# Optimization experiments

Hardware: AMD Instinct MI355X
Metric: run time of the kernel (lower is better)

The kernel has to match this reference:

```python
import jax, jax.numpy as jnp
import numpy as np

N = 100000   # nodes
E = 1600000  # edges
G = 64       # graphs in batch
C = 8        # num_classes
H = 128      # hidden dim


def _lin(k, out_f, in_f):
    return jax.random.normal(k, (out_f, in_f), jnp.float32) * (1.0 / np.sqrt(in_f))


def setup_inputs() -> dict:
    key = jax.random.key(0)
    ks = jax.random.split(key, 16)
    x = jax.random.normal(ks[0], (N, 5), jnp.float32)
    edge_index = jax.random.randint(ks[1], (2, E), 0, N)
    batch = jnp.sort(jax.random.randint(ks[2], (N,), 0, G))
    exinfo = jax.random.normal(ks[3], (G, 10), jnp.float32)
    return {
        "x": x, "edge_index": edge_index, "batch": batch, "exinfo": exinfo,
        # GraphConv1: 3 -> 128 (PyG GraphConv: lin_root(x) + lin_rel(scatter_add(x_j)))
        "Wroot1": _lin(ks[4], H, 3), "Wrel1": _lin(ks[5], H, 3), "brel1": jnp.zeros((H,), jnp.float32),
        # GraphConv2: 128 -> 128
        "Wroot2": _lin(ks[6], H, H), "Wrel2": _lin(ks[7], H, H), "brel2": jnp.zeros((H,), jnp.float32),
        # MLP head
        "W1": _lin(ks[8], 64, 2 * H + 10), "b1": jnp.zeros((64,), jnp.float32),
        "W2": _lin(ks[9], 32, 64), "b2": jnp.zeros((32,), jnp.float32),
        "W3": _lin(ks[10], C, 32), "b3": jnp.zeros((C,), jnp.float32),
    }


def _graph_conv(x, src, dst, Wroot, Wrel, brel):
    # PyG GraphConv (aggr='add'): out_i = Wrel @ sum_{j->i} x_j + brel + Wroot @ x_i
    agg = jax.ops.segment_sum(x[src], dst, num_segments=x.shape[0])  # [N, F]
    return agg @ Wrel.T + brel + x @ Wroot.T


def reference(x, edge_index, batch, exinfo,
              Wroot1, Wrel1, brel1, Wroot2, Wrel2, brel2,
              W1, b1, W2, b2, W3, b3):
    xs = x[:, 2:5]                              # data.x[:, 2:5]
    src, dst = edge_index[0], edge_index[1]
    x1 = jax.nn.relu(_graph_conv(xs, src, dst, Wroot1, Wrel1, brel1))   # [N, 128]
    x2 = jax.nn.relu(_graph_conv(x1, src, dst, Wroot2, Wrel2, brel2))   # [N, 128]
    h = jnp.concatenate([x1, x2], axis=-1)      # [N, 256]
    g = jax.ops.segment_max(h, batch, num_segments=G)  # global max pool [G, 256]
    g = jnp.concatenate([g, exinfo], axis=-1)   # [G, 266]
    g = jax.nn.relu(g @ W1.T + b1)
    g = jax.nn.relu(g @ W2.T + b2)
    return jax.nn.log_softmax(g @ W3.T + b3, axis=-1)
```

## Files before the change

kernel.cpp:

```cpp
#include <hip/hip_runtime.h>

#define N_NODES 100000
#define N_EDGES 1600000
#define NG 64
#define NC 8
#define HD 128

#define BUCKET_SHIFT 8
#define NB ((N_NODES + 255) >> 8)
#define NCHUNK 256
#define EPC (N_EDGES / NCHUNK)

typedef __attribute__((ext_vector_type(8))) __bf16 bf16x8;
typedef __attribute__((ext_vector_type(4))) float f32x4;


__global__ void bin_hist_k(const int* __restrict__ dst, int* __restrict__ hist) {
  __shared__ int lh[NB];
  int c = blockIdx.x, t = threadIdx.x;
  for (int b = t; b < NB; b += 256) lh[b] = 0;
  __syncthreads();
  int e0 = c * EPC;
  for (int i = t; i < EPC; i += 256) atomicAdd(&lh[dst[e0 + i] >> BUCKET_SHIFT], 1);
  __syncthreads();
  for (int b = t; b < NB; b += 256) hist[c * NB + b] = lh[b];
}

__launch_bounds__(512)
__global__ void base_k(const int* __restrict__ hist, int* __restrict__ bucket_base,
                       int* __restrict__ row_ptr) {
  __shared__ int tot[512];
  int t = threadIdx.x;
  int s = 0;
  if (t < NB)
    for (int c = 0; c < NCHUNK; c++) s += hist[c * NB + t];
  tot[t] = s;
  __syncthreads();
  for (int off = 1; off < 512; off <<= 1) {
    int v = (t >= off) ? tot[t - off] : 0;
    __syncthreads();
    tot[t] += v;
    __syncthreads();
  }
  if (t < NB) bucket_base[t] = tot[t] - s;
  if (t == 0) { bucket_base[NB] = N_EDGES; row_ptr[N_NODES] = N_EDGES; }
}

__global__ void chunk_scan_k(int* __restrict__ hist, const int* __restrict__ bucket_base) {
  int b = blockIdx.x, lane = threadIdx.x;
  int carry = bucket_base[b];
#pragma unroll
  for (int it = 0; it < NCHUNK / 64; it++) {
    int c = it * 64 + lane;
    int v = hist[c * NB + b];
    int s = v;
#pragma unroll
    for (int off = 1; off < 64; off <<= 1) {
      int u = __shfl_up(s, off);
      if (lane >= off) s += u;
    }
    hist[c * NB + b] = carry + s - v;
    carry += __shfl(s, 63);
  }
}

__global__ void scatter_k(const int* __restrict__ src, const int* __restrict__ dst,
                          const int* __restrict__ hist, int2* __restrict__ pairs) {
  __shared__ int loff[NB];
  int c = blockIdx.x, t = threadIdx.x;
  for (int b = t; b < NB; b += 256) loff[b] = hist[c * NB + b];
  __syncthreads();
  int e0 = c * EPC;
  for (int i = t; i < EPC; i += 256) {
    int d = dst[e0 + i], s = src[e0 + i];
    int pos = atomicAdd(&loff[d >> BUCKET_SHIFT], 1);
    pairs[pos] = make_int2(d, s);
  }
}

__global__ void bucket_csr_k(const int2* __restrict__ pairs,
                             const int* __restrict__ bucket_base,
                             int* __restrict__ row_ptr, int* __restrict__ csr) {
  __shared__ int cnt[256];
  __shared__ int start[256];
  __shared__ int wsum[4];
  int b = blockIdx.x, t = threadIdx.x, lane = t & 63, wid = t >> 6;
  int nb0 = b << BUCKET_SHIFT;
  int beg = bucket_base[b], end = bucket_base[b + 1];
  cnt[t] = 0;
  __syncthreads();
  for (int i = beg + t; i < end; i += 256) atomicAdd(&cnt[pairs[i].x - nb0], 1);
  __syncthreads();
  int v = cnt[t];
  int s = v;
#pragma unroll
  for (int off = 1; off < 64; off <<= 1) {
    int u = __shfl_up(s, off);
    if (lane >= off) s += u;
  }
  if (lane == 63) wsum[wid] = s;
  __syncthreads();
  if (t == 0) {
    int a = 0;
    for (int j = 0; j < 4; j++) { int x = wsum[j]; wsum[j] = a; a += x; }
  }
  __syncthreads();
  int excl = wsum[wid] + s - v;
  start[t] = excl;
  if (nb0 + t < N_NODES) row_ptr[nb0 + t] = beg + excl;
  cnt[t] = 0;
  __syncthreads();
  for (int i = beg + t; i < end; i += 256) {
    int2 p = pairs[i];
    int li = p.x - nb0;
    int pos = beg + start[li] + atomicAdd(&cnt[li], 1);
    csr[pos] = p.y;
  }
}


__global__ void conv1_k(const float* __restrict__ x, const int* __restrict__ row_ptr,
                        const int* __restrict__ csr, const float* __restrict__ Wroot1,
                        const float* __restrict__ Wrel1, const float* __restrict__ brel1,
                        __bf16* __restrict__ xcat) {
  int node = blockIdx.x * 4 + (threadIdx.x >> 6);
  if (node >= N_NODES) return;
  int lane = threadIdx.x & 63;
  int beg = row_ptr[node], end = row_ptr[node + 1];
  float a0 = 0.f, a1 = 0.f, a2 = 0.f;
  for (int e = beg + lane; e < end; e += 64) {
    int s = csr[e];
    const float* xp = x + (size_t)s * 5;
    a0 += xp[2]; a1 += xp[3]; a2 += xp[4];
  }
#pragma unroll
  for (int m = 1; m < 64; m <<= 1) {
    a0 += __shfl_xor(a0, m);
    a1 += __shfl_xor(a1, m);
    a2 += __shfl_xor(a2, m);
  }
  const float* xn = x + (size_t)node * 5;
  float r0 = xn[2], r1 = xn[3], r2 = xn[4];
  __bf16* orow = xcat + (size_t)node * 256 + 128;
#pragma unroll
  for (int hh = 0; hh < 2; hh++) {
    int h = lane + hh * 64;
    float v = brel1[h]
            + a0 * Wrel1[h * 3 + 0] + a1 * Wrel1[h * 3 + 1] + a2 * Wrel1[h * 3 + 2]
            + r0 * Wroot1[h * 3 + 0] + r1 * Wroot1[h * 3 + 1] + r2 * Wroot1[h * 3 + 2];
    orow[h] = (__bf16)fmaxf(v, 0.f);
  }
}


__global__ void agg2_k(const int* __restrict__ row_ptr, const int* __restrict__ csr,
                       __bf16* xcat) {
  int node = blockIdx.x * 4 + (threadIdx.x >> 6);
  if (node >= N_NODES) return;
  int lane = threadIdx.x & 63;
  int g = lane >> 4, f = lane & 15;
  int beg = row_ptr[node], end = row_ptr[node + 1];
  int deg = end - beg;
  int idx = (lane < deg) ? csr[beg + lane] : 0;
  float acc[8];
#pragma unroll
  for (int k = 0; k < 8; k++) acc[k] = 0.f;
  int dmain = deg < 64 ? deg : 64;
  int j = 0;
  for (; j + 8 <= dmain; j += 8) {
    int s0 = __shfl(idx, j + g);
    int s1 = __shfl(idx, j + 4 + g);
    uint4 u0 = *((const uint4*)(xcat + (size_t)s0 * 256 + 128) + f);
    uint4 u1 = *((const uint4*)(xcat + (size_t)s1 * 256 + 128) + f);
    acc[0] += __uint_as_float(u0.x << 16);  acc[1] += __uint_as_float(u0.x & 0xffff0000u);
    acc[2] += __uint_as_float(u0.y << 16);  acc[3] += __uint_as_float(u0.y & 0xffff0000u);
    acc[4] += __uint_as_float(u0.z << 16);  acc[5] += __uint_as_float(u0.z & 0xffff0000u);
    acc[6] += __uint_as_float(u0.w << 16);  acc[7] += __uint_as_float(u0.w & 0xffff0000u);
    acc[0] += __uint_as_float(u1.x << 16);  acc[1] += __uint_as_float(u1.x & 0xffff0000u);
    acc[2] += __uint_as_float(u1.y << 16);  acc[3] += __uint_as_float(u1.y & 0xffff0000u);
    acc[4] += __uint_as_float(u1.z << 16);  acc[5] += __uint_as_float(u1.z & 0xffff0000u);
    acc[6] += __uint_as_float(u1.w << 16);  acc[7] += __uint_as_float(u1.w & 0xffff0000u);
  }
  for (; j + 4 <= dmain; j += 4) {
    int s0 = __shfl(idx, j + g);
    uint4 u0 = *((const uint4*)(xcat + (size_t)s0 * 256 + 128) + f);
    acc[0] += __uint_as_float(u0.x << 16);  acc[1] += __uint_as_float(u0.x & 0xffff0000u);
    acc[2] += __uint_as_float(u0.y << 16);  acc[3] += __uint_as_float(u0.y & 0xffff0000u);
    acc[4] += __uint_as_float(u0.z << 16);  acc[5] += __uint_as_float(u0.z & 0xffff0000u);
    acc[6] += __uint_as_float(u0.w << 16);  acc[7] += __uint_as_float(u0.w & 0xffff0000u);
  }
  {
    int rem = dmain - j;
    int s0 = __shfl(idx, j + (g < rem ? g : 0));
    if (g < rem) {
      uint4 u0 = *((const uint4*)(xcat + (size_t)s0 * 256 + 128) + f);
      acc[0] += __uint_as_float(u0.x << 16);  acc[1] += __uint_as_float(u0.x & 0xffff0000u);
      acc[2] += __uint_as_float(u0.y << 16);  acc[3] += __uint_as_float(u0.y & 0xffff0000u);
      acc[4] += __uint_as_float(u0.z << 16);  acc[5] += __uint_as_float(u0.z & 0xffff0000u);
      acc[6] += __uint_as_float(u0.w << 16);  acc[7] += __uint_as_float(u0.w & 0xffff0000u);
    }
  }
  for (int e = beg + 64; e < end; e += 4) {
    int m = end - e;
    int s0 = csr[e + (g < m ? g : 0)];
    if (g < m) {
      uint4 u0 = *((const uint4*)(xcat + (size_t)s0 * 256 + 128) + f);
      acc[0] += __uint_as_float(u0.x << 16);  acc[1] += __uint_as_float(u0.x & 0xffff0000u);
      acc[2] += __uint_as_float(u0.y << 16);  acc[3] += __uint_as_float(u0.y & 0xffff0000u);
      acc[4] += __uint_as_float(u0.z << 16);  acc[5] += __uint_as_float(u0.z & 0xffff0000u);
      acc[6] += __uint_as_float(u0.w << 16);  acc[7] += __uint_as_float(u0.w & 0xffff0000u);
    }
  }
#pragma unroll
  for (int k = 0; k < 8; k++) {
    acc[k] += __shfl_xor(acc[k], 16);
    acc[k] += __shfl_xor(acc[k], 32);
  }
  if (g == 0) {
    uint4 o;
    o.x = (__float_as_uint((float)(__bf16)acc[0]) >> 16) | (__float_as_uint((float)(__bf16)acc[1]) & 0xffff0000u);
    o.y = (__float_as_uint((float)(__bf16)acc[2]) >> 16) | (__float_as_uint((float)(__bf16)acc[3]) & 0xffff0000u);
    o.z = (__float_as_uint((float)(__bf16)acc[4]) >> 16) | (__float_as_uint((float)(__bf16)acc[5]) & 0xffff0000u);
    o.w = (__float_as_uint((float)(__bf16)acc[6]) >> 16) | (__float_as_uint((float)(__bf16)acc[7]) & 0xffff0000u);
    *((uint4*)(xcat + (size_t)node * 256) + f) = o;
  }
}


__global__ void build_wc_k(const float* __restrict__ Wrel2, const float* __restrict__ Wroot2,
                           __bf16* __restrict__ Wc) {
  int i = blockIdx.x * 256 + threadIdx.x;
  int h = i >> 8, k = i & 255;
  float v = (k < 128) ? Wrel2[h * 128 + k] : Wroot2[h * 128 + (k - 128)];
  Wc[i] = (__bf16)v;
}


__launch_bounds__(256)
__global__ void gemm2_k(const __bf16* __restrict__ xcat, const __bf16* __restrict__ Wc,
                        const float* __restrict__ brel2, __bf16* __restrict__ x2) {
  int wid = threadIdx.x >> 6, lane = threadIdx.x & 63;
  int nb = (blockIdx.x * 4 + wid) * 32;
  if (nb >= N_NODES) return;
  int r = lane & 15, ko = lane >> 4;
  const __bf16* arow0 = xcat + (size_t)(nb + r) * 256 + ko * 8;
  const __bf16* arow1 = arow0 + 16 * 256;
  const __bf16* brow = Wc + (size_t)r * 256 + ko * 8;
  f32x4 acc0[8], acc1[8];
#pragma unroll
  for (int i = 0; i < 8; i++) {
    acc0[i] = (f32x4){0.f, 0.f, 0.f, 0.f};
    acc1[i] = (f32x4){0.f, 0.f, 0.f, 0.f};
  }
#pragma unroll
  for (int kb = 0; kb < 256; kb += 32) {
    bf16x8 a0 = *(const bf16x8*)(arow0 + kb);
    bf16x8 a1 = *(const bf16x8*)(arow1 + kb);
#pragma unroll
    for (int ht = 0; ht < 8; ht++) {
      bf16x8 b = *(const bf16x8*)(brow + (size_t)ht * 16 * 256 + kb);
      acc0[ht] = __builtin_amdgcn_mfma_f32_16x16x32_bf16(a0, b, acc0[ht], 0, 0, 0);
      acc1[ht] = __builtin_amdgcn_mfma_f32_16x16x32_bf16(a1, b, acc1[ht], 0, 0, 0);
    }
  }
#pragma unroll
  for (int ht = 0; ht < 8; ht++) {
    int h = ht * 16 + r;
    float bias = brel2[h];
#pragma unroll
    for (int rr = 0; rr < 4; rr++) {
      int node = nb + ko * 4 + rr;
      x2[(size_t)node * 128 + h] = (__bf16)fmaxf(acc0[ht][rr] + bias, 0.f);
      x2[(size_t)(node + 16) * 128 + h] = (__bf16)fmaxf(acc1[ht][rr] + bias, 0.f);
    }
  }
}


__global__ void segmax_k(const __bf16* __restrict__ xcat, const __bf16* __restrict__ x2,
                         const int* __restrict__ batch, unsigned int* __restrict__ g) {
  int t = threadIdx.x;
  int n0 = blockIdx.x * 128;
  if (n0 >= N_NODES) return;
  int n1 = n0 + 128 < N_NODES ? n0 + 128 : N_NODES;
  int cur = batch[n0];
  float m = 0.f;
  for (int n = n0; n < n1; n++) {
    int b = batch[n];
    if (b != cur) {
      atomicMax(&g[cur * 256 + t], __float_as_uint(m));
      cur = b; m = 0.f;
    }
    float v = (t < 128) ? (float)xcat[(size_t)n * 256 + 128 + t]
                        : (float)x2[(size_t)n * 128 + (t - 128)];
    m = fmaxf(m, v);
  }
  atomicMax(&g[cur * 256 + t], __float_as_uint(m));
}


__global__ void head1_k(const float* __restrict__ g, const float* __restrict__ exinfo,
                        const float* __restrict__ W1, const float* __restrict__ b1,
                        float* __restrict__ g1) {
  int gg = blockIdx.x;
  int t = threadIdx.x;
  int c = t >> 2, q = t & 3;
  const float* w = W1 + c * 266;
  const float* gr = g + gg * 256;
  float s = 0.f;
  for (int k = q * 64; k < q * 64 + 64; k++) s += gr[k] * w[k];
  if (q == 0) {
    const float* er = exinfo + gg * 10;
    for (int k = 0; k < 10; k++) s += er[k] * w[256 + k];
    s += b1[c];
  }
  s += __shfl_xor(s, 1);
  s += __shfl_xor(s, 2);
  if (q == 0) g1[gg * 64 + c] = fmaxf(s, 0.f);
}

__global__ void head2_k(const float* __restrict__ g1, const float* __restrict__ W2,
                        const float* __restrict__ b2, const float* __restrict__ W3,
                        const float* __restrict__ b3, float* __restrict__ out) {
  __shared__ float s1[64 * 64];
  __shared__ float s2[64 * 32];
  int t = threadIdx.x;
  for (int i = t; i < 4096; i += 256) s1[i] = g1[i];
  __syncthreads();
  for (int o = t; o < 2048; o += 256) {
    int r = o >> 5, c = o & 31;
    float s = b2[c];
    for (int k = 0; k < 64; k++) s += s1[r * 64 + k] * W2[c * 64 + k];
    s2[r * 32 + c] = fmaxf(s, 0.f);
  }
  __syncthreads();
  if (t < 64) {
    float lg[8];
#pragma unroll
    for (int c = 0; c < 8; c++) {
      float s = b3[c];
      for (int k = 0; k < 32; k++) s += s2[t * 32 + k] * W3[c * 32 + k];
      lg[c] = s;
    }
    float mx = lg[0];
#pragma unroll
    for (int c = 1; c < 8; c++) mx = fmaxf(mx, lg[c]);
    float se = 0.f;
#pragma unroll
    for (int c = 0; c < 8; c++) se += expf(lg[c] - mx);
    float lse = mx + logf(se);
#pragma unroll
    for (int c = 0; c < 8; c++) out[t * 8 + c] = lg[c] - lse;
  }
}


extern "C" void kernel_launch(void* const* d_in, const int* in_sizes, int n_in,
                              void* d_out, int out_size, void* d_ws, size_t ws_size,
                              hipStream_t stream) {
  const float* x      = (const float*)d_in[0];
  const int*   edge   = (const int*)d_in[1];
  const int*   batch  = (const int*)d_in[2];
  const float* exinfo = (const float*)d_in[3];
  const float* Wroot1 = (const float*)d_in[4];
  const float* Wrel1  = (const float*)d_in[5];
  const float* brel1  = (const float*)d_in[6];
  const float* Wroot2 = (const float*)d_in[7];
  const float* Wrel2  = (const float*)d_in[8];
  const float* brel2  = (const float*)d_in[9];
  const float* W1     = (const float*)d_in[10];
  const float* b1     = (const float*)d_in[11];
  const float* W2     = (const float*)d_in[12];
  const float* b2     = (const float*)d_in[13];
  const float* W3     = (const float*)d_in[14];
  const float* b3     = (const float*)d_in[15];
  const int* src = edge;
  const int* dst = edge + N_EDGES;

  char* p = (char*)d_ws;
  auto alloc = [&](size_t bytes) {
    char* q = p;
    p += (bytes + 511) & ~(size_t)511;
    return (void*)q;
  };
  __bf16*       Wc          = (__bf16*)alloc(128 * 256 * 2);
  unsigned int* g           = (unsigned int*)alloc(64 * 256 * 4);
  float*        g1          = (float*)alloc(64 * 64 * 4);
  int*          hist        = (int*)alloc((size_t)NCHUNK * NB * 4);
  int*          bucket_base = (int*)alloc((size_t)(NB + 1) * 4);
  int*          row_ptr     = (int*)alloc((size_t)(N_NODES + 1) * 4);
  int*          csr         = (int*)alloc((size_t)N_EDGES * 4);
  __bf16*       xcat        = (__bf16*)alloc((size_t)N_NODES * 256 * 2);
  void*         xp2         = alloc((size_t)N_NODES * 128 * 2);
  int2*         pairs       = (int2*)xp2;
  __bf16*       x2          = (__bf16*)xp2;

  hipMemsetAsync(g, 0, 64 * 256 * 4, stream);
  build_wc_k<<<128, 256, 0, stream>>>(Wrel2, Wroot2, Wc);
  bin_hist_k<<<NCHUNK, 256, 0, stream>>>(dst, hist);
  base_k<<<1, 512, 0, stream>>>(hist, bucket_base, row_ptr);
  chunk_scan_k<<<NB, 64, 0, stream>>>(hist, bucket_base);
  scatter_k<<<NCHUNK, 256, 0, stream>>>(src, dst, hist, pairs);
  bucket_csr_k<<<NB, 256, 0, stream>>>(pairs, bucket_base, row_ptr, csr);
  conv1_k<<<25000, 256, 0, stream>>>(x, row_ptr, csr, Wroot1, Wrel1, brel1, xcat);
  agg2_k<<<25000, 256, 0, stream>>>(row_ptr, csr, xcat);
  gemm2_k<<<782, 256, 0, stream>>>(xcat, Wc, brel2, x2);
  segmax_k<<<782, 256, 0, stream>>>(xcat, x2, batch, g);
  head1_k<<<64, 256, 0, stream>>>((const float*)g, exinfo, W1, b1, g1);
  head2_k<<<1, 256, 0, stream>>>(g1, W2, b2, W3, b3, (float*)d_out);
}
```

Before: 246.4 us.

## Fuse second-layer max-pool into GEMM epilogue and unroll edge gather deeper

The GEMM epilogue for the second GraphConv now applies bias and ReLU and reduces each 32-node tile straight into the per-graph max buffer with atomics. This removes the materialised x2 tensor and its later re-read. A separate segmax kernel now covers only the first-layer half of the features, reading packed bf16 pairs with four node strides per block. The neighbor-aggregation loop is unrolled to four outstanding row loads per iteration to raise memory-level parallelism. The cost is more atomics to global memory when a tile spans a graph boundary, and higher register pressure in the gather.

```diff
diff --git a/kernel.cpp b/kernel.cpp
--- a/kernel.cpp
+++ b/kernel.cpp
@@ -153,6 +153,13 @@
 }
 
 
+#define LDROW(s) (*((const uint4*)(xcat + (size_t)(s) * 256 + 128) + f))
+#define ACC8(u) \
+  acc[0] += __uint_as_float((u).x << 16);  acc[1] += __uint_as_float((u).x & 0xffff0000u); \
+  acc[2] += __uint_as_float((u).y << 16);  acc[3] += __uint_as_float((u).y & 0xffff0000u); \
+  acc[4] += __uint_as_float((u).z << 16);  acc[5] += __uint_as_float((u).z & 0xffff0000u); \
+  acc[6] += __uint_as_float((u).w << 16);  acc[7] += __uint_as_float((u).w & 0xffff0000u);
+
 __global__ void agg2_k(const int* __restrict__ row_ptr, const int* __restrict__ csr,
                        __bf16* xcat) {
   int node = blockIdx.x * 4 + (threadIdx.x >> 6);
@@ -167,48 +174,45 @@
   for (int k = 0; k < 8; k++) acc[k] = 0.f;
   int dmain = deg < 64 ? deg : 64;
   int j = 0;
-  for (; j + 8 <= dmain; j += 8) {
+  for (; j + 16 <= dmain; j += 16) {
     int s0 = __shfl(idx, j + g);
     int s1 = __shfl(idx, j + 4 + g);
-    uint4 u0 = *((const uint4*)(xcat + (size_t)s0 * 256 + 128) + f);
-    uint4 u1 = *((const uint4*)(xcat + (size_t)s1 * 256 + 128) + f);
-    acc[0] += __uint_as_float(u0.x << 16);  acc[1] += __uint_as_float(u0.x & 0xffff0000u);
-    acc[2] += __uint_as_float(u0.y << 16);  acc[3] += __uint_as_float(u0.y & 0xffff0000u);
-    acc[4] += __uint_as_float(u0.z << 16);  acc[5] += __uint_as_float(u0.z & 0xffff0000u);
-    acc[6] += __uint_as_float(u0.w << 16);  acc[7] += __uint_as_float(u0.w & 0xffff0000u);
-    acc[0] += __uint_as_float(u1.x << 16);  acc[1] += __uint_as_float(u1.x & 0xffff0000u);
-    acc[2] += __uint_as_float(u1.y << 16);  acc[3] += __uint_as_float(u1.y & 0xffff0000u);
-    acc[4] += __uint_as_float(u1.z << 16);  acc[5] += __uint_as_float(u1.z & 0xffff0000u);
-    acc[6] += __uint_as_float(u1.w << 16);  acc[7] += __uint_as_float(u1.w & 0xffff0000u);
-  }
-  for (; j + 4 <= dmain; j += 4) {
+    int s2 = __shfl(idx, j + 8 + g);
+    int s3 = __shfl(idx, j + 12 + g);
+    uint4 u0 = LDROW(s0);
+    uint4 u1 = LDROW(s1);
+    uint4 u2 = LDROW(s2);
+    uint4 u3 = LDROW(s3);
+    ACC8(u0) ACC8(u1) ACC8(u2) ACC8(u3)
+  }
+  if (j + 8 <= dmain) {
     int s0 = __shfl(idx, j + g);
-    uint4 u0 = *((const uint4*)(xcat + (size_t)s0 * 256 + 128) + f);
-    acc[0] += __uint_as_float(u0.x << 16);  acc[1] += __uint_as_float(u0.x & 0xffff0000u);
-    acc[2] += __uint_as_float(u0.y << 16);  acc[3] += __uint_as_float(u0.y & 0xffff0000u);
-    acc[4] += __uint_as_float(u0.z << 16);  acc[5] += __uint_as_float(u0.z & 0xffff0000u);
-    acc[6] += __uint_as_float(u0.w << 16);  acc[7] += __uint_as_float(u0.w & 0xffff0000u);
+    int s1 = __shfl(idx, j + 4 + g);
+    uint4 u0 = LDROW(s0);
+    uint4 u1 = LDROW(s1);
+    ACC8(u0) ACC8(u1)
+    j += 8;
+  }
+  if (j + 4 <= dmain) {
+    int s0 = __shfl(idx, j + g);
+    uint4 u0 = LDROW(s0);
+    ACC8(u0)
+    j += 4;
   }
   {
     int rem = dmain - j;
     int s0 = __shfl(idx, j + (g < rem ? g : 0));
     if (g < rem) {
-      uint4 u0 = *((const uint4*)(xcat + (size_t)s0 * 256 + 128) + f);
-      acc[0] += __uint_as_float(u0.x << 16);  acc[1] += __uint_as_float(u0.x & 0xffff0000u);
-      acc[2] += __uint_as_float(u0.y << 16);  acc[3] += __uint_as_float(u0.y & 0xffff0000u);
-      acc[4] += __uint_as_float(u0.z << 16);  acc[5] += __uint_as_float(u0.z & 0xffff0000u);
-      acc[6] += __uint_as_float(u0.w << 16);  acc[7] += __uint_as_float(u0.w & 0xffff0000u);
+      uint4 u0 = LDROW(s0);
+      ACC8(u0)
     }
   }
   for (int e = beg + 64; e < end; e += 4) {
     int m = end - e;
     int s0 = csr[e + (g < m ? g : 0)];
     if (g < m) {
-      uint4 u0 = *((const uint4*)(xcat + (size_t)s0 * 256 + 128) + f);
-      acc[0] += __uint_as_float(u0.x << 16);  acc[1] += __uint_as_float(u0.x & 0xffff0000u);
-      acc[2] += __uint_as_float(u0.y << 16);  acc[3] += __uint_as_float(u0.y & 0xffff0000u);
-      acc[4] += __uint_as_float(u0.z << 16);  acc[5] += __uint_as_float(u0.z & 0xffff0000u);
-      acc[6] += __uint_as_float(u0.w << 16);  acc[7] += __uint_as_float(u0.w & 0xffff0000u);
+      uint4 u0 = LDROW(s0);
+      ACC8(u0)
     }
   }
 #pragma unroll
@@ -238,7 +242,8 @@
 
 __launch_bounds__(256)
 __global__ void gemm2_k(const __bf16* __restrict__ xcat, const __bf16* __restrict__ Wc,
-                        const float* __restrict__ brel2, __bf16* __restrict__ x2) {
+                        const float* __restrict__ brel2, const int* __restrict__ batch,
+                        unsigned int* __restrict__ gout) {
   int wid = threadIdx.x >> 6, lane = threadIdx.x & 63;
   int nb = (blockIdx.x * 4 + wid) * 32;
   if (nb >= N_NODES) return;
@@ -263,39 +268,71 @@
       acc1[ht] = __builtin_amdgcn_mfma_f32_16x16x32_bf16(a1, b, acc1[ht], 0, 0, 0);
     }
   }
-#pragma unroll
-  for (int ht = 0; ht < 8; ht++) {
-    int h = ht * 16 + r;
-    float bias = brel2[h];
+  int gfirst = batch[nb], glast = batch[nb + 31];
+  if (gfirst == glast) {
+    unsigned int* gp = gout + gfirst * 256 + 128;
+#pragma unroll
+    for (int ht = 0; ht < 8; ht++) {
+      float bias = brel2[ht * 16 + r];
+      float m = 0.f;
+#pragma unroll
+      for (int rr = 0; rr < 4; rr++) {
+        m = fmaxf(m, acc0[ht][rr] + bias);
+        m = fmaxf(m, acc1[ht][rr] + bias);
+      }
+      m = fmaxf(m, __shfl_xor(m, 16));
+      m = fmaxf(m, __shfl_xor(m, 32));
+      if (ko == 0) atomicMax(&gp[ht * 16 + r], __float_as_uint(m));
+    }
+  } else {
+    int g0[4], g1[4];
 #pragma unroll
     for (int rr = 0; rr < 4; rr++) {
-      int node = nb + ko * 4 + rr;
-      x2[(size_t)node * 128 + h] = (__bf16)fmaxf(acc0[ht][rr] + bias, 0.f);
-      x2[(size_t)(node + 16) * 128 + h] = (__bf16)fmaxf(acc1[ht][rr] + bias, 0.f);
-    }
-  }
-}
-
-
-__global__ void segmax_k(const __bf16* __restrict__ xcat, const __bf16* __restrict__ x2,
-                         const int* __restrict__ batch, unsigned int* __restrict__ g) {
+      g0[rr] = batch[nb + ko * 4 + rr];
+      g1[rr] = batch[nb + 16 + ko * 4 + rr];
+    }
+#pragma unroll
+    for (int ht = 0; ht < 8; ht++) {
+      int h = ht * 16 + r;
+      float bias = brel2[h];
+#pragma unroll
+      for (int rr = 0; rr < 4; rr++) {
+        atomicMax(&gout[g0[rr] * 256 + 128 + h],
+                  __float_as_uint(fmaxf(acc0[ht][rr] + bias, 0.f)));
+        atomicMax(&gout[g1[rr] * 256 + 128 + h],
+                  __float_as_uint(fmaxf(acc1[ht][rr] + bias, 0.f)));
+      }
+    }
+  }
+}
+
+
+__global__ void segmax1_k(const __bf16* __restrict__ xcat, const int* __restrict__ batch,
+                          unsigned int* __restrict__ g) {
   int t = threadIdx.x;
-  int n0 = blockIdx.x * 128;
-  if (n0 >= N_NODES) return;
-  int n1 = n0 + 128 < N_NODES ? n0 + 128 : N_NODES;
-  int cur = batch[n0];
-  float m = 0.f;
-  for (int n = n0; n < n1; n++) {
+  int f = t & 63;
+  int s = t >> 6;
+  int n0 = blockIdx.x * 256;
+  float m0 = 0.f, m1 = 0.f;
+  int cur = -1;
+  int n1 = n0 + 256 < N_NODES ? n0 + 256 : N_NODES;
+  for (int n = n0 + s; n < n1; n += 4) {
     int b = batch[n];
     if (b != cur) {
-      atomicMax(&g[cur * 256 + t], __float_as_uint(m));
-      cur = b; m = 0.f;
-    }
-    float v = (t < 128) ? (float)xcat[(size_t)n * 256 + 128 + t]
-                        : (float)x2[(size_t)n * 128 + (t - 128)];
-    m = fmaxf(m, v);
-  }
-  atomicMax(&g[cur * 256 + t], __float_as_uint(m));
+      if (cur >= 0) {
+        atomicMax(&g[cur * 256 + 2 * f], __float_as_uint(m0));
+        atomicMax(&g[cur * 256 + 2 * f + 1], __float_as_uint(m1));
+      }
+      cur = b; m0 = 0.f; m1 = 0.f;
+    }
+    unsigned int u = ((const unsigned int*)(xcat + (size_t)n * 256 + 128))[f];
+    m0 = fmaxf(m0, __uint_as_float(u << 16));
+    m1 = fmaxf(m1, __uint_as_float(u & 0xffff0000u));
+  }
+  if (cur >= 0) {
+    atomicMax(&g[cur * 256 + 2 * f], __float_as_uint(m0));
+    atomicMax(&g[cur * 256 + 2 * f + 1], __float_as_uint(m1));
+  }
 }
 
 
@@ -391,9 +428,7 @@
   int*          row_ptr     = (int*)alloc((size_t)(N_NODES + 1) * 4);
   int*          csr         = (int*)alloc((size_t)N_EDGES * 4);
   __bf16*       xcat        = (__bf16*)alloc((size_t)N_NODES * 256 * 2);
-  void*         xp2         = alloc((size_t)N_NODES * 128 * 2);
-  int2*         pairs       = (int2*)xp2;
-  __bf16*       x2          = (__bf16*)xp2;
+  int2*         pairs       = (int2*)alloc((size_t)N_EDGES * 8);
 
   hipMemsetAsync(g, 0, 64 * 256 * 4, stream);
   build_wc_k<<<128, 256, 0, stream>>>(Wrel2, Wroot2, Wc);
@@ -404,8 +439,8 @@
   bucket_csr_k<<<NB, 256, 0, stream>>>(pairs, bucket_base, row_ptr, csr);
   conv1_k<<<25000, 256, 0, stream>>>(x, row_ptr, csr, Wroot1, Wrel1, brel1, xcat);
   agg2_k<<<25000, 256, 0, stream>>>(row_ptr, csr, xcat);
-  gemm2_k<<<782, 256, 0, stream>>>(xcat, Wc, brel2, x2);
-  segmax_k<<<782, 256, 0, stream>>>(xcat, x2, batch, g);
+  gemm2_k<<<782, 256, 0, stream>>>(xcat, Wc, brel2, batch, g);
+  segmax1_k<<<NB, 256, 0, stream>>>(xcat, batch, g);
   head1_k<<<64, 256, 0, stream>>>((const float*)g, exinfo, W1, b1, g1);
   head2_k<<<1, 256, 0, stream>>>(g1, W2, b2, W3, b3, (float*)d_out);
 }
```

New measurement: 249.2 us. About the same (+1.1%).
